# Optimization experiments

Measured on AMD Instinct MI355X. Metric: run time of the kernel, lower is better.

## Reference

```python
import jax, jax.numpy as jnp
import numpy as np

ALPHA_POS, ALPHA_NEG, GAMMA, TAU = 1.0, 2.0, 2.0, 0.7
LAMBDA_CP, MU_ECE, N_BINS = 6.0, 5.0, 15
N = 16777216


def setup_inputs() -> dict:
    key = jax.random.key(0)
    k1, k2, k3 = jax.random.split(key, 3)
    p_hat = jax.random.uniform(k1, (N,), dtype=jnp.float32)
    u_hat = jax.random.uniform(k2, (N,), dtype=jnp.float32)
    targets = jax.random.randint(k3, (N,), 0, 2, dtype=jnp.int32)
    return {"p_hat": p_hat, "u_hat": u_hat, "targets": targets}


def _ece(probs, labels):
    # bin b covers (b/n_bins, (b+1)/n_bins]; single-pass histogram via segment_sum
    bins = jnp.clip(jnp.ceil(probs * N_BINS).astype(jnp.int32) - 1, 0, N_BINS - 1)
    sum_p = jax.ops.segment_sum(probs, bins, num_segments=N_BINS)
    sum_y = jax.ops.segment_sum(labels, bins, num_segments=N_BINS)
    # (|I_b|/N)*|mean_y - mean_p| == |sum_y - sum_p| / N ; empty bins contribute 0
    n = probs.shape[0]
    return jnp.sum(jnp.abs(sum_y - sum_p)) / n


def reference(p_hat, u_hat, targets):
    t = targets.astype(p_hat.dtype)
    pos = targets == 1
    pt = jnp.where(pos, p_hat, 1.0 - p_hat)
    alpha = jnp.where(pos, ALPHA_POS, ALPHA_NEG)
    focal = jnp.mean(-alpha * (1.0 - pt) ** GAMMA * jnp.log(pt + 1e-12))

    mask_ow = (~pos) & (p_hat > TAU)   # overconfident wrong
    mask_uc = pos & (p_hat < TAU)      # underconfident correct
    penalty = jnp.where(mask_ow, (1.0 - u_hat) ** 2,
                        jnp.where(mask_uc, u_hat ** 2, 0.0))
    cp_loss = jnp.mean(penalty)

    ece = _ece(p_hat, t)
    return focal + LAMBDA_CP * cp_loss + MU_ECE * ece
```

## Files before the change

### kernel.cpp

```cpp
#include <hip/hip_runtime.h>

#define NB 15
#define NV 17
#define GRID 1024
#define BLOCK 256


__device__ __forceinline__ void process_elem(float pk, float uk, int tk,
                                             float& facc, float& cacc,
                                             float* bins)
{
    bool pos = (tk == 1);

    float pt    = pos ? pk : 1.0f - pk;
    float alpha = pos ? 1.0f : 2.0f;
    float om    = 1.0f - pt;
    facc -= alpha * om * om * __logf(pt + 1e-12f);

    float w   = 1.0f - uk;
    float pen = pos ? ((pk < 0.7f) ? uk * uk : 0.0f)
                    : ((pk > 0.7f) ? w * w : 0.0f);
    cacc += pen;

    int b = (int)ceilf(pk * 15.0f) - 1;
    b = (b < 0) ? 0 : ((b > NB - 1) ? NB - 1 : b);
    float v = (pos ? 1.0f : 0.0f) - pk;
    #pragma unroll
    for (int j = 0; j < NB; ++j)
        bins[j] += (b == j) ? v : 0.0f;
}

__global__ __launch_bounds__(BLOCK) void fcl_main(
    const float* __restrict__ p_hat,
    const float* __restrict__ u_hat,
    const int*   __restrict__ targets,
    float* __restrict__ partials,
    int n4, int n)
{
    float bins[NB];
    #pragma unroll
    for (int j = 0; j < NB; ++j) bins[j] = 0.0f;
    float facc = 0.0f, cacc = 0.0f;

    const float4* __restrict__ p4 = (const float4*)p_hat;
    const float4* __restrict__ u4 = (const float4*)u_hat;
    const int4*   __restrict__ t4 = (const int4*)targets;

    const int stride = gridDim.x * blockDim.x;
    int i = blockIdx.x * blockDim.x + threadIdx.x;

    for (; i + stride < n4; i += 2 * stride) {
        float4 p0 = p4[i];          float4 p1 = p4[i + stride];
        float4 u0 = u4[i];          float4 u1 = u4[i + stride];
        int4   t0 = t4[i];          int4   t1 = t4[i + stride];
        #pragma unroll
        for (int k = 0; k < 4; ++k)
            process_elem((&p0.x)[k], (&u0.x)[k], (&t0.x)[k], facc, cacc, bins);
        #pragma unroll
        for (int k = 0; k < 4; ++k)
            process_elem((&p1.x)[k], (&u1.x)[k], (&t1.x)[k], facc, cacc, bins);
    }
    if (i < n4) {
        float4 p0 = p4[i]; float4 u0 = u4[i]; int4 t0 = t4[i];
        #pragma unroll
        for (int k = 0; k < 4; ++k)
            process_elem((&p0.x)[k], (&u0.x)[k], (&t0.x)[k], facc, cacc, bins);
    }

    if (blockIdx.x == 0 && threadIdx.x == 0) {
        for (int j = n4 * 4; j < n; ++j)
            process_elem(p_hat[j], u_hat[j], targets[j], facc, cacc, bins);
    }

    float vals[NV];
    vals[0] = facc; vals[1] = cacc;
    #pragma unroll
    for (int j = 0; j < NB; ++j) vals[2 + j] = bins[j];

    #pragma unroll
    for (int off = 32; off > 0; off >>= 1) {
        #pragma unroll
        for (int j = 0; j < NV; ++j)
            vals[j] += __shfl_down(vals[j], off, 64);
    }

    __shared__ float lds[BLOCK / 64][NV];
    const int wave = threadIdx.x >> 6;
    const int lane = threadIdx.x & 63;
    if (lane == 0) {
        #pragma unroll
        for (int j = 0; j < NV; ++j) lds[wave][j] = vals[j];
    }
    __syncthreads();

    if (threadIdx.x < NV) {
        float s = 0.0f;
        #pragma unroll
        for (int w = 0; w < BLOCK / 64; ++w) s += lds[w][threadIdx.x];
        partials[threadIdx.x * gridDim.x + blockIdx.x] = s;
    }
}

__global__ __launch_bounds__(1024) void fcl_final(
    const float* __restrict__ partials,
    float* __restrict__ out, float inv_n, int grid)
{
    const int t = threadIdx.x;
    float v[NV];
    #pragma unroll
    for (int j = 0; j < NV; ++j) v[j] = partials[j * grid + t];

    #pragma unroll
    for (int off = 32; off > 0; off >>= 1) {
        #pragma unroll
        for (int j = 0; j < NV; ++j)
            v[j] += __shfl_down(v[j], off, 64);
    }

    __shared__ float lds[16][NV];
    const int wave = t >> 6;
    const int lane = t & 63;
    if (lane == 0) {
        #pragma unroll
        for (int j = 0; j < NV; ++j) lds[wave][j] = v[j];
    }
    __syncthreads();

    if (t == 0) {
        float s[NV];
        #pragma unroll
        for (int j = 0; j < NV; ++j) s[j] = 0.0f;
        for (int w = 0; w < 16; ++w)
            #pragma unroll
            for (int j = 0; j < NV; ++j) s[j] += lds[w][j];
        float e = 0.0f;
        #pragma unroll
        for (int b = 0; b < NB; ++b) e += fabsf(s[2 + b]);
        out[0] = (s[0] + 6.0f * s[1] + 5.0f * e) * inv_n;
    }
}

extern "C" void kernel_launch(void* const* d_in, const int* in_sizes, int n_in,
                              void* d_out, int out_size, void* d_ws, size_t ws_size,
                              hipStream_t stream) {
    const float* p = (const float*)d_in[0];
    const float* u = (const float*)d_in[1];
    const int*   t = (const int*)d_in[2];
    float* out = (float*)d_out;
    float* ws  = (float*)d_ws;

    const int n  = in_sizes[0];
    const int n4 = n / 4;

    fcl_main<<<GRID, BLOCK, 0, stream>>>(p, u, t, ws, n4, n);
    fcl_final<<<1, 1024, 0, stream>>>(ws, out, 1.0f / (float)n, GRID);
}
```

Before: 204.7 us.

## Move per-thread ECE bins to LDS with atomic adds and double the grid

Per-thread histogram bins move out of registers (a 15-way predicated select-add per element) into a private LDS slot per thread, updated with atomicAdd at the computed bin index. The main grid grows to 2048 blocks when the workspace is large enough, and the final kernel loops so it can reduce more than 1024 partials. The focal term is rewritten slightly to drop the alpha multiply. The LDS atomics, with stride-15 per-thread slots, may add latency and bank conflicts in exchange for fewer ALU ops and lower register pressure.

```diff
diff --git a/kernel.cpp b/kernel.cpp
--- a/kernel.cpp
+++ b/kernel.cpp
@@ -2,20 +2,21 @@
 
 #define NB 15
 #define NV 17
-#define GRID 1024
 #define BLOCK 256
+#define BIGGRID 2048
 
 
 __device__ __forceinline__ void process_elem(float pk, float uk, int tk,
                                              float& facc, float& cacc,
-                                             float* bins)
+                                             float* __restrict__ hbp)
 {
     bool pos = (tk == 1);
 
-    float pt    = pos ? pk : 1.0f - pk;
-    float alpha = pos ? 1.0f : 2.0f;
-    float om    = 1.0f - pt;
-    facc -= alpha * om * om * __logf(pt + 1e-12f);
+    float pt = pos ? pk : 1.0f - pk;
+    float om = 1.0f - pt;
+    float l  = __logf(pt + 1e-12f);
+    float f  = om * om * l;
+    facc -= pos ? f : 2.0f * f;
 
     float w   = 1.0f - uk;
     float pen = pos ? ((pk < 0.7f) ? uk * uk : 0.0f)
@@ -25,9 +26,7 @@
     int b = (int)ceilf(pk * 15.0f) - 1;
     b = (b < 0) ? 0 : ((b > NB - 1) ? NB - 1 : b);
     float v = (pos ? 1.0f : 0.0f) - pk;
-    #pragma unroll
-    for (int j = 0; j < NB; ++j)
-        bins[j] += (b == j) ? v : 0.0f;
+    atomicAdd(hbp + b, v);
 }
 
 __global__ __launch_bounds__(BLOCK) void fcl_main(
@@ -37,9 +36,14 @@
     float* __restrict__ partials,
     int n4, int n)
 {
-    float bins[NB];
+    __shared__ float hb[BLOCK * NB];
+    __shared__ float lds[BLOCK / 64][NV];
+
+    const int tb = threadIdx.x * NB;
+    float* hbp = &hb[tb];
     #pragma unroll
-    for (int j = 0; j < NB; ++j) bins[j] = 0.0f;
+    for (int j = 0; j < NB; ++j) hbp[j] = 0.0f;
+
     float facc = 0.0f, cacc = 0.0f;
 
     const float4* __restrict__ p4 = (const float4*)p_hat;
@@ -55,27 +59,27 @@
         int4   t0 = t4[i];          int4   t1 = t4[i + stride];
         #pragma unroll
         for (int k = 0; k < 4; ++k)
-            process_elem((&p0.x)[k], (&u0.x)[k], (&t0.x)[k], facc, cacc, bins);
+            process_elem((&p0.x)[k], (&u0.x)[k], (&t0.x)[k], facc, cacc, hbp);
         #pragma unroll
         for (int k = 0; k < 4; ++k)
-            process_elem((&p1.x)[k], (&u1.x)[k], (&t1.x)[k], facc, cacc, bins);
+            process_elem((&p1.x)[k], (&u1.x)[k], (&t1.x)[k], facc, cacc, hbp);
     }
     if (i < n4) {
         float4 p0 = p4[i]; float4 u0 = u4[i]; int4 t0 = t4[i];
         #pragma unroll
         for (int k = 0; k < 4; ++k)
-            process_elem((&p0.x)[k], (&u0.x)[k], (&t0.x)[k], facc, cacc, bins);
+            process_elem((&p0.x)[k], (&u0.x)[k], (&t0.x)[k], facc, cacc, hbp);
     }
 
     if (blockIdx.x == 0 && threadIdx.x == 0) {
         for (int j = n4 * 4; j < n; ++j)
-            process_elem(p_hat[j], u_hat[j], targets[j], facc, cacc, bins);
+            process_elem(p_hat[j], u_hat[j], targets[j], facc, cacc, hbp);
     }
 
     float vals[NV];
     vals[0] = facc; vals[1] = cacc;
     #pragma unroll
-    for (int j = 0; j < NB; ++j) vals[2 + j] = bins[j];
+    for (int j = 0; j < NB; ++j) vals[2 + j] = hbp[j];
 
     #pragma unroll
     for (int off = 32; off > 0; off >>= 1) {
@@ -84,7 +88,6 @@
             vals[j] += __shfl_down(vals[j], off, 64);
     }
 
-    __shared__ float lds[BLOCK / 64][NV];
     const int wave = threadIdx.x >> 6;
     const int lane = threadIdx.x & 63;
     if (lane == 0) {
@@ -108,7 +111,12 @@
     const int t = threadIdx.x;
     float v[NV];
     #pragma unroll
-    for (int j = 0; j < NV; ++j) v[j] = partials[j * grid + t];
+    for (int j = 0; j < NV; ++j) {
+        float s = 0.0f;
+        for (int g = t; g < grid; g += 1024)
+            s += partials[j * grid + g];
+        v[j] = s;
+    }
 
     #pragma unroll
     for (int off = 32; off > 0; off >>= 1) {
@@ -152,6 +160,8 @@
     const int n  = in_sizes[0];
     const int n4 = n / 4;
 
-    fcl_main<<<GRID, BLOCK, 0, stream>>>(p, u, t, ws, n4, n);
-    fcl_final<<<1, 1024, 0, stream>>>(ws, out, 1.0f / (float)n, GRID);
+    const int grid = (ws_size >= (size_t)(NV * BIGGRID) * sizeof(float)) ? BIGGRID : 1024;
+
+    fcl_main<<<grid, BLOCK, 0, stream>>>(p, u, t, ws, n4, n);
+    fcl_final<<<1, 1024, 0, stream>>>(ws, out, 1.0f / (float)n, grid);
 }
```

After: 241.0 us. 1.18x slower.
